# Kernel tuning notes

Hardware: AMD Instinct MI355X
Metric: run time of the kernel (lower is better)

Reference implementation:

```python
import jax, jax.numpy as jnp
import numpy as np

N_NODES = 100000
N_EDGES = 400000
F_IN = 128
HID = 128
HEADS = 4
N_GRAPHS = 2000
NEG_SLOPE = 0.2  # GATConv leaky relu slope
BN_EPS = 1e-5


def setup_inputs() -> dict:
    key = jax.random.key(0)
    ks = jax.random.split(key, 20)
    s = 0.05
    d = {}
    d["x"] = jax.random.normal(ks[0], (N_NODES, F_IN), jnp.float32)
    d["edge_index"] = jax.random.randint(ks[1], (2, N_EDGES), 0, N_NODES, jnp.int32)
    d["batch"] = jnp.sort(jax.random.randint(ks[2], (N_NODES,), 0, N_GRAPHS, jnp.int32))
    # GCN stack (first layer in=F_IN==HID so stackable)
    d["gcn_W"] = jax.random.normal(ks[3], (3, HID, HID), jnp.float32) * s
    d["gcn_b"] = jax.random.normal(ks[4], (3, HID), jnp.float32) * s
    # BatchNorm (eval mode: running stats)
    d["bn_gamma"] = jnp.ones((3, HID), jnp.float32)
    d["bn_beta"] = jnp.zeros((3, HID), jnp.float32)
    d["bn_mean"] = jax.random.normal(ks[5], (3, HID), jnp.float32) * s
    d["bn_var"] = jax.random.uniform(ks[6], (3, HID), jnp.float32, 0.5, 1.5)
    # GAT (heads=4, concat=False -> mean over heads)
    d["gat_W"] = jax.random.normal(ks[7], (HID, HEADS * HID), jnp.float32) * s
    d["gat_att_src"] = jax.random.normal(ks[8], (HEADS, HID), jnp.float32) * s
    d["gat_att_dst"] = jax.random.normal(ks[9], (HEADS, HID), jnp.float32) * s
    d["gat_b"] = jax.random.normal(ks[10], (HID,), jnp.float32) * s
    # classifier 128 -> 64 -> 32 -> 1
    d["c1_W"] = jax.random.normal(ks[11], (HID, HID // 2), jnp.float32) * s
    d["c1_b"] = jnp.zeros((HID // 2,), jnp.float32)
    d["c2_W"] = jax.random.normal(ks[12], (HID // 2, HID // 4), jnp.float32) * s
    d["c2_b"] = jnp.zeros((HID // 4,), jnp.float32)
    d["c3_W"] = jax.random.normal(ks[13], (HID // 4, 1), jnp.float32) * s
    d["c3_b"] = jnp.zeros((1,), jnp.float32)
    return d


def reference(x, edge_index, batch, gcn_W, gcn_b, bn_gamma, bn_beta, bn_mean, bn_var,
              gat_W, gat_att_src, gat_att_dst, gat_b,
              c1_W, c1_b, c2_W, c2_b, c3_W, c3_b):
    N = x.shape[0]
    loops = jnp.arange(N, dtype=edge_index.dtype)
    src = jnp.concatenate([edge_index[0], loops])  # messages flow src -> dst
    dst = jnp.concatenate([edge_index[1], loops])

    # GCN symmetric normalization with self loops
    deg = jax.ops.segment_sum(jnp.ones_like(dst, jnp.float32), dst, N)
    dinv = jnp.where(deg > 0, jax.lax.rsqrt(deg), 0.0)
    enorm = (dinv[src] * dinv[dst])[:, None]  # [E+N, 1]

    h = x
    for i in range(3):
        t = h @ gcn_W[i]                                   # [N, HID]
        agg = jax.ops.segment_sum(t[src] * enorm, dst, N) + gcn_b[i]
        agg = (agg - bn_mean[i]) * jax.lax.rsqrt(bn_var[i] + BN_EPS) * bn_gamma[i] + bn_beta[i]
        agg = jax.nn.relu(agg)
        h = h + agg if i > 0 else agg                      # residual from layer 1

    # GAT, heads=4, concat=False (mean over heads), with self loops
    hh = (h @ gat_W).reshape(N, HEADS, HID)
    a_s = jnp.einsum('nhd,hd->nh', hh, gat_att_src)
    a_d = jnp.einsum('nhd,hd->nh', hh, gat_att_dst)
    e = jax.nn.leaky_relu(a_s[src] + a_d[dst], NEG_SLOPE)  # [E+N, HEADS]
    emax = jax.ops.segment_max(e, dst, N)                  # every node has a self loop
    ex = jnp.exp(e - emax[dst])
    denom = jax.ops.segment_sum(ex, dst, N)
    alpha = ex / (denom[dst] + 1e-16)
    att = jax.ops.segment_sum(hh[src] * alpha[:, :, None], dst, N)  # [N, HEADS, HID]
    h = h + (att.mean(axis=1) + gat_b)

    # global mean pool over graphs
    gsum = jax.ops.segment_sum(h, batch, N_GRAPHS)
    cnt = jax.ops.segment_sum(jnp.ones((N, 1), jnp.float32), batch, N_GRAPHS)
    g = gsum / jnp.maximum(cnt, 1.0)

    z = jax.nn.relu(g @ c1_W + c1_b)
    z = jax.nn.relu(z @ c2_W + c2_b)
    return z @ c3_W + c3_b  # [N_GRAPHS, 1]
```

## Files before the change

### kernel.cpp

```cpp
#include <hip/hip_runtime.h>
#include <math.h>

#define NN 100000
#define NE 400000
#define HID 128
#define HEADS 4
#define NG 2000
#define BN_EPS 1e-5f
#define NEG_SLOPE 0.2f
#define NB_SCAN 391

__global__ void k_fill(float* __restrict__ p, float v, long n) {
    long i = (long)blockIdx.x * blockDim.x + threadIdx.x;
    if (i < n) p[i] = v;
}

__global__ void k_zero_i(int* __restrict__ p, int n) {
    int i = blockIdx.x * blockDim.x + threadIdx.x;
    if (i < n) p[i] = 0;
}

__global__ void k_count(const int* __restrict__ dst, int* __restrict__ cnt) {
    int e = blockIdx.x * blockDim.x + threadIdx.x;
    if (e < NE) atomicAdd(&cnt[dst[e]], 1);
}

__global__ void k_dinv2(const int* __restrict__ cnt, float* __restrict__ dinv) {
    int n = blockIdx.x * blockDim.x + threadIdx.x;
    if (n < NN) dinv[n] = rsqrtf((float)cnt[n] + 1.0f);
}

__global__ __launch_bounds__(256) void k_bsum(const int* __restrict__ cnt, int* __restrict__ bsum) {
    __shared__ int s[256];
    int tid = threadIdx.x;
    int n = blockIdx.x * 256 + tid;
    s[tid] = (n < NN) ? cnt[n] : 0;
    __syncthreads();
    for (int off = 128; off > 0; off >>= 1) {
        if (tid < off) s[tid] += s[tid + off];
        __syncthreads();
    }
    if (tid == 0) bsum[blockIdx.x] = s[0];
}

__global__ __launch_bounds__(512) void k_bscan(int* __restrict__ bsum, int* __restrict__ row_ptr) {
    __shared__ int s[512];
    int tid = threadIdx.x;
    int v = (tid < NB_SCAN) ? bsum[tid] : 0;
    s[tid] = v;
    __syncthreads();
    for (int off = 1; off < 512; off <<= 1) {
        int t_ = (tid >= off) ? s[tid - off] : 0;
        __syncthreads();
        s[tid] += t_;
        __syncthreads();
    }
    if (tid < NB_SCAN) bsum[tid] = s[tid] - v;
    if (tid == 0) row_ptr[NN] = NE;
}

__global__ __launch_bounds__(256) void k_rowptr(const int* __restrict__ cnt, const int* __restrict__ boff,
                                                int* __restrict__ row_ptr) {
    __shared__ int s[256];
    int tid = threadIdx.x;
    int n = blockIdx.x * 256 + tid;
    int v = (n < NN) ? cnt[n] : 0;
    s[tid] = v;
    __syncthreads();
    for (int off = 1; off < 256; off <<= 1) {
        int t_ = (tid >= off) ? s[tid - off] : 0;
        __syncthreads();
        s[tid] += t_;
        __syncthreads();
    }
    if (n < NN) row_ptr[n] = boff[blockIdx.x] + s[tid] - v;
}

__global__ void k_csr(const int* __restrict__ src, const int* __restrict__ dst,
                      const int* __restrict__ row_ptr, int* __restrict__ fill,
                      const float* __restrict__ dinv,
                      int* __restrict__ csr_src, float* __restrict__ csr_w) {
    int e = blockIdx.x * blockDim.x + threadIdx.x;
    if (e >= NE) return;
    int s = src[e], d = dst[e];
    int pos = row_ptr[d] + atomicAdd(&fill[d], 1);
    csr_src[pos] = s;
    csr_w[pos] = dinv[s] * dinv[d];
}

__global__ __launch_bounds__(512) void k_gemm128(const float* __restrict__ A,
                                                 const float* __restrict__ W,
                                                 float* __restrict__ C,
                                                 int nrows, int ldw, int coffW,
                                                 const float* __restrict__ att_s,
                                                 const float* __restrict__ att_d,
                                                 float* __restrict__ as_out,
                                                 float* __restrict__ ad_out) {
    __shared__ float Ws[64][128];
    __shared__ float As[128][64];
    int tid = threadIdx.x;
    int row0 = blockIdx.x * 128;
    int c0 = (tid & 31) * 4;
    int r0 = (tid >> 5) * 8;
    float acc[8][4] = {};
    for (int kb = 0; kb < 2; ++kb) {
        __syncthreads();
        for (int i = tid; i < 2048; i += 512) {
            int k  = i >> 5;
            int c4 = (i & 31) * 4;
            *(float4*)&Ws[k][c4] =
                *(const float4*)&W[(long)(kb * 64 + k) * ldw + coffW + c4];
        }
        for (int i = tid; i < 2048; i += 512) {
            int r  = i >> 4;
            int k4 = (i & 15) * 4;
            int gr = row0 + r;
            float4 v = (gr < nrows)
                ? *(const float4*)&A[(long)gr * 128 + kb * 64 + k4]
                : make_float4(0.f, 0.f, 0.f, 0.f);
            *(float4*)&As[r][k4] = v;
        }
        __syncthreads();
        for (int k = 0; k < 64; ++k) {
            float4 wv = *(const float4*)&Ws[k][c0];
#pragma unroll
            for (int j = 0; j < 8; ++j) {
                float a = As[r0 + j][k];
                acc[j][0] += a * wv.x;
                acc[j][1] += a * wv.y;
                acc[j][2] += a * wv.z;
                acc[j][3] += a * wv.w;
            }
        }
    }
#pragma unroll
    for (int j = 0; j < 8; ++j) {
        int gr = row0 + r0 + j;
        if (gr < nrows)
            *(float4*)&C[(long)gr * 128 + c0] =
                make_float4(acc[j][0], acc[j][1], acc[j][2], acc[j][3]);
    }
    if (att_s) {
#pragma unroll
        for (int j = 0; j < 8; ++j) {
            float ps = acc[j][0] * att_s[c0] + acc[j][1] * att_s[c0 + 1]
                     + acc[j][2] * att_s[c0 + 2] + acc[j][3] * att_s[c0 + 3];
            float pd = acc[j][0] * att_d[c0] + acc[j][1] * att_d[c0 + 1]
                     + acc[j][2] * att_d[c0 + 2] + acc[j][3] * att_d[c0 + 3];
#pragma unroll
            for (int off = 16; off > 0; off >>= 1) {
                ps += __shfl_down(ps, off, 32);
                pd += __shfl_down(pd, off, 32);
            }
            int gr = row0 + r0 + j;
            if ((tid & 31) == 0 && gr < nrows) { as_out[gr] = ps; ad_out[gr] = pd; }
        }
    }
}

__global__ __launch_bounds__(128) void k_gcn_agg(const float* __restrict__ t,
                                                 const int* __restrict__ row_ptr,
                                                 const int* __restrict__ csr_src,
                                                 const float* __restrict__ csr_w,
                                                 const float* __restrict__ dinv,
                                                 const float* __restrict__ b,
                                                 const float* __restrict__ gamma,
                                                 const float* __restrict__ beta,
                                                 const float* __restrict__ mean,
                                                 const float* __restrict__ var,
                                                 float* __restrict__ h, int residual) {
    int n = blockIdx.x;
    int d = threadIdx.x;
    int e0 = row_ptr[n], e1 = row_ptr[n + 1];
    float dn = dinv[n];
    float acc = t[(long)n * HID + d] * dn * dn;
    for (int j = e0; j < e1; ++j)
        acc += t[(long)csr_src[j] * HID + d] * csr_w[j];
    float v = acc + b[d];
    v = (v - mean[d]) * rsqrtf(var[d] + BN_EPS) * gamma[d] + beta[d];
    v = fmaxf(v, 0.f);
    long idx = (long)n * HID + d;
    h[idx] = residual ? (h[idx] + v) : v;
}

__global__ __launch_bounds__(128) void k_gat_agg(const float* __restrict__ t,
                                                 const int* __restrict__ row_ptr,
                                                 const int* __restrict__ csr_src,
                                                 const float* __restrict__ a_s,
                                                 const float* __restrict__ a_d,
                                                 const float* __restrict__ gat_b,
                                                 float* __restrict__ agg,
                                                 float* __restrict__ h, int mode) {
    int n = blockIdx.x;
    int d = threadIdx.x;
    int e0 = row_ptr[n], e1 = row_ptr[n + 1];
    float adn = a_d[n];
    float es = a_s[n] + adn;
    es = (es > 0.f) ? es : NEG_SLOPE * es;
    float m = es;
    for (int j = e0; j < e1; ++j) {
        float e = a_s[csr_src[j]] + adn;
        e = (e > 0.f) ? e : NEG_SLOPE * e;
        m = fmaxf(m, e);
    }
    float w0 = expf(es - m);
    float denom = w0;
    float acc = t[(long)n * HID + d] * w0;
    for (int j = e0; j < e1; ++j) {
        int s = csr_src[j];
        float e = a_s[s] + adn;
        e = (e > 0.f) ? e : NEG_SLOPE * e;
        float w = expf(e - m);
        denom += w;
        acc += t[(long)s * HID + d] * w;
    }
    acc = 0.25f * acc / (denom + 1e-16f);
    long idx = (long)n * HID + d;
    if (mode == 0)      agg[idx] = acc;
    else if (mode == 1) agg[idx] += acc;
    else                h[idx] += agg[idx] + acc + gat_b[d];
}

__global__ void k_pool(const float* __restrict__ h, const int* __restrict__ batch,
                       float* __restrict__ gsum, float* __restrict__ cnt) {
    long idx = (long)blockIdx.x * blockDim.x + threadIdx.x;
    if (idx >= (long)NN * HID) return;
    int n = (int)(idx >> 7);
    int d = (int)(idx & 127);
    int g = batch[n];
    atomicAdd(&gsum[(long)g * HID + d], h[idx]);
    if (d == 0) atomicAdd(&cnt[g], 1.f);
}

__global__ void k_gdiv(float* __restrict__ gsum, const float* __restrict__ cnt) {
    long idx = (long)blockIdx.x * blockDim.x + threadIdx.x;
    if (idx >= (long)NG * HID) return;
    int g = (int)(idx >> 7);
    gsum[idx] /= fmaxf(cnt[g], 1.f);
}

__global__ __launch_bounds__(64) void k_cls1(const float* __restrict__ g, const float* __restrict__ W,
                                             const float* __restrict__ b, float* __restrict__ z) {
    int gi = blockIdx.x;
    int j = threadIdx.x;
    float acc = b[j];
    for (int d = 0; d < 128; ++d) acc += g[(long)gi * 128 + d] * W[d * 64 + j];
    z[(long)gi * 64 + j] = fmaxf(acc, 0.f);
}

__global__ __launch_bounds__(64) void k_cls2(const float* __restrict__ z1, const float* __restrict__ W,
                                             const float* __restrict__ b, float* __restrict__ z) {
    int gi = blockIdx.x * 2 + (threadIdx.x >> 5);
    int j = threadIdx.x & 31;
    if (gi >= NG) return;
    float acc = b[j];
    for (int d = 0; d < 64; ++d) acc += z1[(long)gi * 64 + d] * W[d * 32 + j];
    z[(long)gi * 32 + j] = fmaxf(acc, 0.f);
}

__global__ void k_cls3(const float* __restrict__ z2, const float* __restrict__ W,
                       const float* __restrict__ b, float* __restrict__ out) {
    int gi = blockIdx.x * blockDim.x + threadIdx.x;
    if (gi >= NG) return;
    float acc = b[0];
    for (int d = 0; d < 32; ++d) acc += z2[(long)gi * 32 + d] * W[d];
    out[gi] = acc;
}

extern "C" void kernel_launch(void* const* d_in, const int* in_sizes, int n_in,
                              void* d_out, int out_size, void* d_ws, size_t ws_size,
                              hipStream_t stream) {
    const float* x     = (const float*)d_in[0];
    const int*   ei    = (const int*)d_in[1];
    const int*   src   = ei;
    const int*   dst   = ei + NE;
    const int*   batch = (const int*)d_in[2];
    const float* gcn_W = (const float*)d_in[3];
    const float* gcn_b = (const float*)d_in[4];
    const float* bn_g  = (const float*)d_in[5];
    const float* bn_be = (const float*)d_in[6];
    const float* bn_m  = (const float*)d_in[7];
    const float* bn_v  = (const float*)d_in[8];
    const float* gat_W = (const float*)d_in[9];
    const float* att_s = (const float*)d_in[10];
    const float* att_d = (const float*)d_in[11];
    const float* gat_b = (const float*)d_in[12];
    const float* c1W = (const float*)d_in[13];
    const float* c1b = (const float*)d_in[14];
    const float* c2W = (const float*)d_in[15];
    const float* c2b = (const float*)d_in[16];
    const float* c3W = (const float*)d_in[17];
    const float* c3b = (const float*)d_in[18];
    float* out = (float*)d_out;

    float* ws = (float*)d_ws;
    size_t o = 0;
    float* dinv    = ws + o; o += NN;
    int*   cnt     = (int*)(ws + o); o += NN;
    int*   bsum    = (int*)(ws + o); o += 512;
    int*   row_ptr = (int*)(ws + o); o += NN + 1;
    int*   csr_src = (int*)(ws + o); o += NE;
    float* csr_w   = ws + o; o += NE;
    float* h       = ws + o; o += (size_t)NN * HID;
    float* t       = ws + o; o += (size_t)NN * HID;
    float* agg     = ws + o; o += (size_t)NN * HID;
    float* a_s     = ws + o; o += NN;
    float* a_d     = ws + o; o += NN;
    float* gsum    = ws + o; o += (size_t)NG * HID;
    float* cntg    = ws + o; o += NG;
    float* z1      = ws + o; o += (size_t)NG * 64;
    float* z2      = ws + o; o += (size_t)NG * 32;

    auto cdiv = [](long a, long b) { return (int)((a + b - 1) / b); };

    k_zero_i<<<cdiv(NN, 256), 256, 0, stream>>>(cnt, NN);
    k_count<<<cdiv(NE, 256), 256, 0, stream>>>(dst, cnt);
    k_dinv2<<<cdiv(NN, 256), 256, 0, stream>>>(cnt, dinv);
    k_bsum<<<NB_SCAN, 256, 0, stream>>>(cnt, bsum);
    k_bscan<<<1, 512, 0, stream>>>(bsum, row_ptr);
    k_rowptr<<<NB_SCAN, 256, 0, stream>>>(cnt, bsum, row_ptr);
    k_zero_i<<<cdiv(NN, 256), 256, 0, stream>>>(cnt, NN);
    k_csr<<<cdiv(NE, 256), 256, 0, stream>>>(src, dst, row_ptr, cnt, dinv, csr_src, csr_w);

    const float* hin = x;
    for (int L = 0; L < 3; ++L) {
        k_gemm128<<<cdiv(NN, 128), 512, 0, stream>>>(hin, gcn_W + (size_t)L * HID * HID, t,
                                                     NN, HID, 0, nullptr, nullptr, nullptr, nullptr);
        k_gcn_agg<<<NN, 128, 0, stream>>>(t, row_ptr, csr_src, csr_w, dinv,
                                          gcn_b + L * HID, bn_g + L * HID, bn_be + L * HID,
                                          bn_m + L * HID, bn_v + L * HID, h, L > 0);
        hin = h;
    }

    for (int hd = 0; hd < HEADS; ++hd) {
        k_gemm128<<<cdiv(NN, 128), 512, 0, stream>>>(h, gat_W, t, NN, HEADS * HID, hd * HID,
                                                     att_s + hd * HID, att_d + hd * HID, a_s, a_d);
        k_gat_agg<<<NN, 128, 0, stream>>>(t, row_ptr, csr_src, a_s, a_d, gat_b, agg, h,
                                          hd == 0 ? 0 : (hd == HEADS - 1 ? 2 : 1));
    }

    k_fill<<<cdiv((long)(NG * HID + NG), 256), 256, 0, stream>>>(gsum, 0.f, (long)(NG * HID + NG));
    k_pool<<<cdiv((long)NN * HID, 256), 256, 0, stream>>>(h, batch, gsum, cntg);
    k_gdiv<<<cdiv((long)NG * HID, 256), 256, 0, stream>>>(gsum, cntg);
    k_cls1<<<NG, 64, 0, stream>>>(gsum, c1W, c1b, z1);
    k_cls2<<<NG / 2, 64, 0, stream>>>(z1, c2W, c2b, z2);
    k_cls3<<<cdiv(NG, 256), 256, 0, stream>>>(z2, c3W, c3b, out);
}
```

Baseline: 1.339 ms.

## Fuse pooling and classifier into one kernel; vectorize GEMM A-tile LDS reads

Measured after the change: 1.347 ms. About the same (+0.6%).

```diff
diff --git a/kernel.cpp b/kernel.cpp
--- a/kernel.cpp
+++ b/kernel.cpp
@@ -9,11 +9,6 @@
 #define BN_EPS 1e-5f
 #define NEG_SLOPE 0.2f
 #define NB_SCAN 391
-
-__global__ void k_fill(float* __restrict__ p, float v, long n) {
-    long i = (long)blockIdx.x * blockDim.x + threadIdx.x;
-    if (i < n) p[i] = v;
-}
 
 __global__ void k_zero_i(int* __restrict__ p, int n) {
     int i = blockIdx.x * blockDim.x + threadIdx.x;
@@ -121,15 +116,21 @@
             *(float4*)&As[r][k4] = v;
         }
         __syncthreads();
-        for (int k = 0; k < 64; ++k) {
-            float4 wv = *(const float4*)&Ws[k][c0];
-#pragma unroll
-            for (int j = 0; j < 8; ++j) {
-                float a = As[r0 + j][k];
-                acc[j][0] += a * wv.x;
-                acc[j][1] += a * wv.y;
-                acc[j][2] += a * wv.z;
-                acc[j][3] += a * wv.w;
+        for (int k4 = 0; k4 < 64; k4 += 4) {
+            float4 a4[8];
+#pragma unroll
+            for (int j = 0; j < 8; ++j) a4[j] = *(const float4*)&As[r0 + j][k4];
+#pragma unroll
+            for (int i = 0; i < 4; ++i) {
+                float4 wv = *(const float4*)&Ws[k4 + i][c0];
+#pragma unroll
+                for (int j = 0; j < 8; ++j) {
+                    float a = (i == 0) ? a4[j].x : (i == 1) ? a4[j].y : (i == 2) ? a4[j].z : a4[j].w;
+                    acc[j][0] += a * wv.x;
+                    acc[j][1] += a * wv.y;
+                    acc[j][2] += a * wv.z;
+                    acc[j][3] += a * wv.w;
+                }
             }
         }
     }
@@ -221,50 +222,47 @@
     else                h[idx] += agg[idx] + acc + gat_b[d];
 }
 
-__global__ void k_pool(const float* __restrict__ h, const int* __restrict__ batch,
-                       float* __restrict__ gsum, float* __restrict__ cnt) {
-    long idx = (long)blockIdx.x * blockDim.x + threadIdx.x;
-    if (idx >= (long)NN * HID) return;
-    int n = (int)(idx >> 7);
-    int d = (int)(idx & 127);
-    int g = batch[n];
-    atomicAdd(&gsum[(long)g * HID + d], h[idx]);
-    if (d == 0) atomicAdd(&cnt[g], 1.f);
-}
-
-__global__ void k_gdiv(float* __restrict__ gsum, const float* __restrict__ cnt) {
-    long idx = (long)blockIdx.x * blockDim.x + threadIdx.x;
-    if (idx >= (long)NG * HID) return;
-    int g = (int)(idx >> 7);
-    gsum[idx] /= fmaxf(cnt[g], 1.f);
-}
-
-__global__ __launch_bounds__(64) void k_cls1(const float* __restrict__ g, const float* __restrict__ W,
-                                             const float* __restrict__ b, float* __restrict__ z) {
-    int gi = blockIdx.x;
-    int j = threadIdx.x;
-    float acc = b[j];
-    for (int d = 0; d < 128; ++d) acc += g[(long)gi * 128 + d] * W[d * 64 + j];
-    z[(long)gi * 64 + j] = fmaxf(acc, 0.f);
-}
-
-__global__ __launch_bounds__(64) void k_cls2(const float* __restrict__ z1, const float* __restrict__ W,
-                                             const float* __restrict__ b, float* __restrict__ z) {
-    int gi = blockIdx.x * 2 + (threadIdx.x >> 5);
-    int j = threadIdx.x & 31;
-    if (gi >= NG) return;
-    float acc = b[j];
-    for (int d = 0; d < 64; ++d) acc += z1[(long)gi * 64 + d] * W[d * 32 + j];
-    z[(long)gi * 32 + j] = fmaxf(acc, 0.f);
-}
-
-__global__ void k_cls3(const float* __restrict__ z2, const float* __restrict__ W,
-                       const float* __restrict__ b, float* __restrict__ out) {
-    int gi = blockIdx.x * blockDim.x + threadIdx.x;
-    if (gi >= NG) return;
-    float acc = b[0];
-    for (int d = 0; d < 32; ++d) acc += z2[(long)gi * 32 + d] * W[d];
-    out[gi] = acc;
+__global__ __launch_bounds__(128) void k_pool_cls(const float* __restrict__ h,
+                                                  const int* __restrict__ batch,
+                                                  const float* __restrict__ c1W,
+                                                  const float* __restrict__ c1b,
+                                                  const float* __restrict__ c2W,
+                                                  const float* __restrict__ c2b,
+                                                  const float* __restrict__ c3W,
+                                                  const float* __restrict__ c3b,
+                                                  float* __restrict__ out) {
+    int g = blockIdx.x;
+    int tid = threadIdx.x;
+    int lo = 0, hb = NN;
+    while (lo < hb) { int mid = (lo + hb) >> 1; if (batch[mid] < g) lo = mid + 1; else hb = mid; }
+    int a = lo, b2 = NN;
+    while (a < b2) { int mid = (a + b2) >> 1; if (batch[mid] < g + 1) a = mid + 1; else b2 = mid; }
+    int hi = a;
+    float s = 0.f;
+    for (int n = lo; n < hi; ++n) s += h[(long)n * HID + tid];
+    __shared__ float gbuf[HID];
+    __shared__ float z1buf[64];
+    __shared__ float z2buf[32];
+    gbuf[tid] = s / fmaxf((float)(hi - lo), 1.f);
+    __syncthreads();
+    if (tid < 64) {
+        float acc = c1b[tid];
+        for (int d2 = 0; d2 < 128; ++d2) acc += gbuf[d2] * c1W[d2 * 64 + tid];
+        z1buf[tid] = fmaxf(acc, 0.f);
+    }
+    __syncthreads();
+    if (tid < 32) {
+        float acc = c2b[tid];
+        for (int d2 = 0; d2 < 64; ++d2) acc += z1buf[d2] * c2W[d2 * 32 + tid];
+        z2buf[tid] = fmaxf(acc, 0.f);
+    }
+    __syncthreads();
+    if (tid < 32) {
+        float p = z2buf[tid] * c3W[tid];
+#pragma unroll
+        for (int off = 16; off > 0; off >>= 1) p += __shfl_down(p, off, 32);
+        if (tid == 0) out[g] = p + c3b[0];
+    }
 }
 
 extern "C" void kernel_launch(void* const* d_in, const int* in_sizes, int n_in,
@@ -306,10 +304,6 @@
     float* agg     = ws + o; o += (size_t)NN * HID;
     float* a_s     = ws + o; o += NN;
     float* a_d     = ws + o; o += NN;
-    float* gsum    = ws + o; o += (size_t)NG * HID;
-    float* cntg    = ws + o; o += NG;
-    float* z1      = ws + o; o += (size_t)NG * 64;
-    float* z2      = ws + o; o += (size_t)NG * 32;
 
     auto cdiv = [](long a, long b) { return (int)((a + b - 1) / b); };
 
@@ -339,10 +333,5 @@
                                           hd == 0 ? 0 : (hd == HEADS - 1 ? 2 : 1));
     }
 
-    k_fill<<<cdiv((long)(NG * HID + NG), 256), 256, 0, stream>>>(gsum, 0.f, (long)(NG * HID + NG));
-    k_pool<<<cdiv((long)NN * HID, 256), 256, 0, stream>>>(h, batch, gsum, cntg);
-    k_gdiv<<<cdiv((long)NG * HID, 256), 256, 0, stream>>>(gsum, cntg);
-    k_cls1<<<NG, 64, 0, stream>>>(gsum, c1W, c1b, z1);
-    k_cls2<<<NG / 2, 64, 0, stream>>>(z1, c2W, c2b, z2);
-    k_cls3<<<cdiv(NG, 256), 256, 0, stream>>>(z2, c3W, c3b, out);
-}
+    k_pool_cls<<<NG, 128, 0, stream>>>(h, batch, c1W, c1b, c2W, c2b, c3W, c3b, out);
+}
```
